# Kernel tuning notes

Hardware: AMD Instinct MI355X
Metric: run time of the kernel (lower is better)

Reference implementation:

```python
import jax, jax.numpy as jnp
import numpy as np

N_NODES = 200000
N_EDGES = 800000
D_IN = 64
D_OUT = 64
NUM_RELATIONS = 16
NUM_BASES = 8


def setup_inputs() -> dict:
    key = jax.random.key(0)
    k_x, k_s, k_t, k_r, k_b, k_a = jax.random.split(key, 6)
    x = jax.random.normal(k_x, (N_NODES, D_IN), dtype=jnp.float32)
    node_keep_mask = jnp.ones((N_NODES,), dtype=bool)
    source = jax.random.randint(k_s, (N_EDGES,), 0, N_NODES, dtype=jnp.int64)
    target = jax.random.randint(k_t, (N_EDGES,), 0, N_NODES, dtype=jnp.int64)
    edge_type = jax.random.randint(k_r, (N_EDGES,), 0, NUM_RELATIONS, dtype=jnp.int64)
    # parameters: xavier-normal bases, L1-normalized attention coefficients
    std = float(np.sqrt(2.0 / (D_IN + D_OUT)))
    bases = jax.random.normal(k_b, (NUM_BASES, D_IN, D_OUT), dtype=jnp.float32) * std
    att = jax.random.uniform(k_a, (NUM_RELATIONS + 1, NUM_BASES), dtype=jnp.float32)
    att = att / jnp.sum(jnp.abs(att), axis=1, keepdims=True)
    return {"x": x, "node_keep_mask": node_keep_mask, "source": source,
            "target": target, "edge_type": edge_type, "bases": bases, "att": att}


def reference(x, node_keep_mask, source, target, edge_type, bases, att):
    num_relations = att.shape[0] - 1
    # per-node, per-basis transformed features: (N, B, D_out)
    t = jnp.einsum('nd,bde->nbe', x, bases)
    # self-loop term (att row num_relations), masked by node_keep_mask
    self_msg = jnp.einsum('nbe,b->ne', t, att[num_relations])
    out = jnp.where(node_keep_mask[:, None], self_msg, jnp.zeros((), dtype=x.dtype))
    # per-node, per-relation messages: (N, R, D_out) -- collapses the per-relation
    # python loop of the original into one contraction
    h = jnp.einsum('nbe,rb->nre', t, att[:num_relations])
    # bidirectional edges (original concatenates [src,tgt] and [tgt,src])
    src2 = jnp.concatenate([source, target])
    tgt2 = jnp.concatenate([target, source])
    et2 = jnp.concatenate([edge_type, edge_type])
    m = h[src2, et2]  # (2E, D_out) gather
    out = out.at[tgt2].add(m)  # scatter-add over edges
    return out
```

## Files before the change

kernel.cpp:

```cpp
#include <hip/hip_runtime.h>
#include <hip/hip_bf16.h>
#include <stdint.h>
#include <stddef.h>

#define N_NODES 200000
#define N_EDGES 800000
#define NREL 16
#define NBASES 8

typedef __attribute__((ext_vector_type(8))) short short8b;
typedef __attribute__((ext_vector_type(4))) float float4v;
typedef __attribute__((ext_vector_type(4))) int int4v;

__device__ __forceinline__ short f32_bf16(float f) {
  uint32_t u = __builtin_bit_cast(uint32_t, f);
  uint32_t r = u + 0x7FFFu + ((u >> 16) & 1u);
  return (short)(uint16_t)(r >> 16);
}
__device__ __forceinline__ uint16_t f32_bf16_hw(float f) {
  __hip_bfloat16 h = __float2bfloat16(f);
  return __builtin_bit_cast(uint16_t, h);
}
__device__ __forceinline__ float bf2f(uint16_t h) {
  return __builtin_bit_cast(float, (uint32_t)h << 16);
}

__global__ __launch_bounds__(256) void k_wprep(const float* __restrict__ bases,
                                               const float* __restrict__ att,
                                               uint16_t* __restrict__ Wt) {
  int i = blockIdx.x * 256 + threadIdx.x;
  if (i >= 17 * 64 * 64) return;
  int r = i >> 12;
  int e = (i >> 6) & 63;
  int d = i & 63;
  float acc = 0.f;
  for (int b = 0; b < NBASES; ++b)
    acc += att[r * NBASES + b] * bases[b * 4096 + d * 64 + e];
  Wt[i] = (uint16_t)f32_bf16(acc);
}

#define MAXTILES 112528
#define MAXRECS  (MAXTILES * 16)
#define NB 196
#define CNT_BLOCKS  782
#define CAST_BLOCKS 6250
#define PREP_BLOCKS 440
#define WS_CNTR    0
#define WS_GCUR2   128
#define WS_RSTART  256
#define WS_GCUR    384
#define WS_WT      512
#define WS_TILEREL 139776
#define WS_VSTART  1052416
#define WS_CNTT    1852416
#define WS_RECS    2652416
#define WS_MSG     17056128
#define WS_TOTAL   (WS_MSG + (size_t)MAXRECS * 128)
#define TR_RELOFF  WS_MSG
#define TR_NOFF    (TR_RELOFF + 3200000)
#define TR_ESLOT   (TR_NOFF + 800000)
#define TR_SCRATCH (TR_ESLOT + 6400000)
#define TR_H       (TR_SCRATCH + 6400000)
#define TR_BASE    (TR_H + 613088)
#define TR_REGS    (TR_BASE + 613088)

__global__ __launch_bounds__(256) void k_init(const float* __restrict__ bases,
                                              const float* __restrict__ att,
                                              uint16_t* __restrict__ Wt,
                                              int* __restrict__ zero0) {
  int b = blockIdx.x;
  int tid = threadIdx.x;
  if (b < 273) {
    int i = b * 256 + tid;
    if (i < 17 * 64 * 64) {
      int r = i >> 12;
      int e = (i >> 6) & 63;
      int d = i & 63;
      float acc = 0.f;
      for (int bb = 0; bb < NBASES; ++bb)
        acc += att[r * NBASES + bb] * bases[bb * 4096 + d * 64 + e];
      Wt[i] = (uint16_t)f32_bf16(acc);
    }
  } else {
    if (tid < 128) zero0[tid] = 0;
  }
}

__global__ __launch_bounds__(256) void k_count(const int* __restrict__ src,
                                               const int* __restrict__ tgt,
                                               const int* __restrict__ et,
                                               const int* __restrict__ mask,
                                               int* __restrict__ cntr,
                                               int* __restrict__ H,
                                               int* __restrict__ reloff,
                                               int* __restrict__ noff,
                                               const float* __restrict__ x,
                                               uint16_t* __restrict__ xb,
                                               int nE, int nN) {
  int b = blockIdx.x;
  int tid = threadIdx.x;
  if (b >= CNT_BLOCKS) {
    int i = (b - CNT_BLOCKS) * 256 + tid;
    const float* xp = x + (size_t)i * 8;
    float4v q0 = __builtin_nontemporal_load((const float4v*)xp);
    float4v q1 = __builtin_nontemporal_load((const float4v*)(xp + 4));
    short8b o;
    o[0] = f32_bf16_hw(q0[0]); o[1] = f32_bf16_hw(q0[1]); o[2] = f32_bf16_hw(q0[2]); o[3] = f32_bf16_hw(q0[3]);
    o[4] = f32_bf16_hw(q1[0]); o[5] = f32_bf16_hw(q1[1]); o[6] = f32_bf16_hw(q1[2]); o[7] = f32_bf16_hw(q1[3]);
    *(short8b*)(xb + (size_t)i * 8) = o;
    return;
  }
  __shared__ int lh[NREL + 1], lbase[NREL + 1];
  __shared__ int bh[NB];
  if (tid <= NREL) lh[tid] = 0;
  if (tid < NB) bh[tid] = 0;
  __syncthreads();
  int base = b * 1024 + tid;
  bool isE[4], isN[4];
  int r4[4], loff[4], loffN[4];
#pragma unroll
  for (int k = 0; k < 4; ++k) {
    int i = base + k * 256;
    isE[k] = i < nE;
    isN[k] = (i < nN) && mask[i];
    if (isE[k]) {
      r4[k] = et[i];
      int s_ = src[i], t_ = tgt[i];
      loff[k] = atomicAdd(&lh[r4[k]], 2);
      atomicAdd(&bh[t_ >> 10], 1);
      atomicAdd(&bh[s_ >> 10], 1);
    }
    if (isN[k]) loffN[k] = atomicAdd(&lh[NREL], 1);
  }
  __syncthreads();
  if (tid <= NREL)
    lbase[tid] = lh[tid] ? atomicAdd(&cntr[tid], lh[tid]) : 0;
  if (tid < NB) H[b * NB + tid] = bh[tid];
  __syncthreads();
#pragma unroll
  for (int k = 0; k < 4; ++k) {
    int i = base + k * 256;
    if (isE[k]) __builtin_nontemporal_store(lbase[r4[k]] + loff[k], reloff + i);
    if (isN[k]) __builtin_nontemporal_store(lbase[NREL] + loffN[k], noff + i);
  }
}

__global__ __launch_bounds__(256) void k_base(const int* __restrict__ H,
                                              int* __restrict__ baseM,
                                              int* __restrict__ regStart,
                                              int* __restrict__ regTot,
                                              int* __restrict__ gcur2,
                                              const int* __restrict__ cntr,
                                              int* __restrict__ rstart_g,
                                              uint8_t* __restrict__ tileRel,
                                              int2* __restrict__ recs,
                                              int maxTiles) {
  int tid = threadIdx.x;
  if (blockIdx.x >= NB) {
    int bp = blockIdx.x - NB;
    __shared__ int s[NREL + 2];
    if (tid == 0) {
      int base = 0;
      for (int r = 0; r <= NREL; ++r) {
        s[r] = base;
        base = (base + cntr[r] + 15) & ~15;
      }
      s[NREL + 1] = base;
    }
    __syncthreads();
    if (bp == 0) {
      if (tid <= NREL + 1) rstart_g[tid] = s[tid];
      for (int w = tid; w < (NREL + 1) * 16; w += 256) {
        int r = w >> 4, j = w & 15;
        int pos = s[r] + cntr[r] + j;
        if (pos < s[r + 1]) recs[pos] = make_int2(-1, -1);
      }
    }
    int t = bp * 256 + tid;
    if (t < maxTiles) {
      int p = t * 16;
      uint8_t rr = 255;
      if (p < s[NREL + 1]) {
        int q = 0;
        for (int k = 1; k <= NREL; ++k)
          if (p >= s[k]) q = k;
        rr = (uint8_t)q;
      }
      tileRel[t] = rr;
    }
    return;
  }
  int b = blockIdx.x;
  int lane = tid & 63, wid = tid >> 6;
  int vals[4]; int ts = 0;
#pragma unroll
  for (int k = 0; k < 4; ++k) {
    int idx = tid * 4 + k;
    vals[k] = (idx < CNT_BLOCKS) ? H[idx * NB + b] : 0;
    ts += vals[k];
  }
  int incl = ts;
  for (int off = 1; off < 64; off <<= 1) {
    int n = __shfl_up(incl, off, 64);
    if (lane >= off) incl += n;
  }
  __shared__ int wsum[4];
  __shared__ int s_start;
  if (lane == 63) wsum[wid] = incl;
  __syncthreads();
  if (tid == 0) {
    int t0 = wsum[0], t1 = wsum[1], t2 = wsum[2], t3 = wsum[3];
    int tot = t0 + t1 + t2 + t3;
    int st = atomicAdd(gcur2, tot);
    regStart[b] = st;
    regTot[b] = tot;
    s_start = st;
    wsum[0] = 0; wsum[1] = t0; wsum[2] = t0 + t1; wsum[3] = t0 + t1 + t2;
  }
  __syncthreads();
  int run = s_start + wsum[wid] + incl - ts;
#pragma unroll
  for (int k = 0; k < 4; ++k) {
    int idx = tid * 4 + k;
    if (idx < CNT_BLOCKS) {
      baseM[idx * NB + b] = run;
      run += vals[k];
    }
  }
}

__global__ __launch_bounds__(256) void k_scat(const int* __restrict__ src,
                                              const int* __restrict__ tgt,
                                              const int* __restrict__ baseM,
                                              int* __restrict__ scratch,
                                              int nE) {
  int b = blockIdx.x;
  int tid = threadIdx.x;
  __shared__ int bh[NB];
  __shared__ int bb[NB];
  if (tid < NB) { bh[tid] = 0; bb[tid] = baseM[b * NB + tid]; }
  __syncthreads();
#pragma unroll
  for (int k = 0; k < 4; ++k) {
    int i = b * 1024 + k * 256 + tid;
    if (i < nE) {
      int t_ = tgt[i], s_ = src[i];
      int offT = atomicAdd(&bh[t_ >> 10], 1);
      scratch[bb[t_ >> 10] + offT] = ((t_ & 1023) << 21) | (2 * i);
      int offS = atomicAdd(&bh[s_ >> 10], 1);
      scratch[bb[s_ >> 10] + offS] = ((s_ & 1023) << 21) | (2 * i + 1);
    }
  }
}

__global__ __launch_bounds__(256) void k_slot(const int* __restrict__ scratch,
                                              const int* __restrict__ regStart,
                                              const int* __restrict__ regTot,
                                              const int* __restrict__ mask,
                                              const int* __restrict__ noff,
                                              const int* __restrict__ rstart,
                                              int* __restrict__ eslot,
                                              int* __restrict__ vstart,
                                              int* __restrict__ cntt,
                                              int* __restrict__ gcur,
                                              int2* __restrict__ recs,
                                              int nN) {
  int b = blockIdx.x;
  int tid = threadIdx.x;
  __shared__ int cnt[1024];
  __shared__ int sabs[1024];
  __shared__ int wsum[4];
  __shared__ int s_base, s_rs16;
#pragma unroll
  for (int k = 0; k < 4; ++k) cnt[tid + k * 256] = 0;
  if (tid == 0) s_rs16 = rstart[NREL];
  __syncthreads();
  int start = regStart[b];
  int tot = regTot[b];
  for (int it = tid; it < tot; it += 256)
    atomicAdd(&cnt[scratch[start + it] >> 21], 1);
  __syncthreads();
  int lane = tid & 63, wid = tid >> 6;
  int vals[4]; int ts = 0;
#pragma unroll
  for (int k = 0; k < 4; ++k) {
    int j = tid * 4 + k;
    int v = b * 1024 + j;
    int m = (v < nN) ? (mask[v] ? 1 : 0) : 0;
    vals[k] = cnt[j] + m;
    ts += vals[k];
  }
  int incl = ts;
  for (int off = 1; off < 64; off <<= 1) {
    int n = __shfl_up(incl, off, 64);
    if (lane >= off) incl += n;
  }
  if (lane == 63) wsum[wid] = incl;
  __syncthreads();
  if (tid == 0) {
    int t0 = wsum[0], t1 = wsum[1], t2 = wsum[2], t3 = wsum[3];
    s_base = atomicAdd(gcur, t0 + t1 + t2 + t3);
    wsum[0] = 0; wsum[1] = t0; wsum[2] = t0 + t1; wsum[3] = t0 + t1 + t2;
  }
  __syncthreads();
  int run = s_base + wsum[wid] + incl - ts;
#pragma unroll
  for (int k = 0; k < 4; ++k) {
    int j = tid * 4 + k;
    sabs[j] = run;
    int v = b * 1024 + j;
    if (v < nN) { vstart[v] = run; cntt[v] = vals[k]; }
    run += vals[k];
  }
  __syncthreads();
  for (int it = tid; it < tot; it += 256) {
    int rec = scratch[start + it];
    int slot = atomicAdd(&sabs[rec >> 21], 1);
    eslot[rec & 0x1FFFFF] = slot;
  }
  __syncthreads();
#pragma unroll
  for (int k = 0; k < 4; ++k) {
    int j = tid * 4 + k;
    int v = b * 1024 + j;
    if (v < nN && mask[v])
      recs[s_rs16 + noff[v]] = make_int2(v, sabs[j]);
  }
}

__global__ __launch_bounds__(256) void k_write(const int* __restrict__ src,
                                               const int* __restrict__ tgt,
                                               const int* __restrict__ et,
                                               const int* __restrict__ reloff,
                                               const int* __restrict__ eslot,
                                               const int* __restrict__ rstart,
                                               int2* __restrict__ recs,
                                               int nE) {
  __shared__ int s_rs[NREL + 1];
  if (threadIdx.x <= NREL) s_rs[threadIdx.x] = rstart[threadIdx.x];
  __syncthreads();
  int i = blockIdx.x * 256 + threadIdx.x;
  if (i < nE) {
    int r = et[i];
    int rl = __builtin_nontemporal_load(reloff + i);
    long long ev = __builtin_nontemporal_load((const long long*)(eslot + 2 * i));
    int s1 = (int)(ev & 0xFFFFFFFFll);
    int s2 = (int)(ev >> 32);
    int s_ = src[i], t_ = tgt[i];
    int pos = s_rs[r] + rl;
    *(int4*)(recs + pos) = make_int4(s_, s1, t_, s2);
  }
}

__global__ __launch_bounds__(256) void k_phaseA(const uint16_t* __restrict__ xb,
                                                const int2* __restrict__ recs,
                                                const uint16_t* __restrict__ Wt,
                                                const uint8_t* __restrict__ tileRel,
                                                uint16_t* __restrict__ msg,
                                                int ntiles) {
  __shared__ uint16_t s_m[4][2][16 * 72];
  __shared__ int s_slot[4][2][16];
  const int wid = threadIdx.x >> 6;
  const int lane = threadIdx.x & 63;
  const int quad = lane >> 4;
  const int m16 = lane & 15;
  const int t0 = (blockIdx.x * 4 + wid) * 4;

  if (tileRel[t0] == 255) return;

  int rel4[4];
#pragma unroll
  for (int it = 0; it < 4; ++it) {
    int t = t0 + it;
    rel4[it] = (t < ntiles) ? (int)tileRel[t] : 255;
  }
  int2 rec4[4];
#pragma unroll
  for (int it = 0; it < 4; ++it) {
    if (rel4[it] != 255) {
      long long rv = __builtin_nontemporal_load((const long long*)(recs + (t0 + it) * 16 + m16));
      rec4[it].x = (int)(rv & 0xFFFFFFFFll);
      rec4[it].y = (int)(rv >> 32);
    } else {
      rec4[it] = make_int2(-1, -1);
    }
  }
  short8b a0_[4], a1_[4];
#pragma unroll
  for (int it = 0; it < 4; ++it) {
    int u = rec4[it].x < 0 ? 0 : rec4[it].x;
    const uint16_t* xp = xb + (size_t)u * 64 + quad * 8;
    a0_[it] = *(const short8b*)(xp);
    a1_[it] = *(const short8b*)(xp + 32);
  }

  int curRel = -1;
  short8b bfrag[4][2] = {};

#pragma unroll
  for (int it = 0; it < 4; ++it) {
    int rel = rel4[it];
    if (rel == 255) continue;
    int par = it & 1;

    if (rel != curRel) {
      curRel = rel;
      const uint16_t* wbase = Wt + (size_t)rel * 4096;
      for (int nt = 0; nt < 4; ++nt)
        for (int kt = 0; kt < 2; ++kt)
          bfrag[nt][kt] = *(const short8b*)(wbase + (size_t)(nt * 16 + m16) * 64 + kt * 32 + quad * 8);
    }

    float4v acc[4];
    for (int nt = 0; nt < 4; ++nt) { acc[nt][0] = 0.f; acc[nt][1] = 0.f; acc[nt][2] = 0.f; acc[nt][3] = 0.f; }
    for (int nt = 0; nt < 4; ++nt) {
      acc[nt] = __builtin_amdgcn_mfma_f32_16x16x32_bf16(a0_[it], bfrag[nt][0], acc[nt], 0, 0, 0);
      acc[nt] = __builtin_amdgcn_mfma_f32_16x16x32_bf16(a1_[it], bfrag[nt][1], acc[nt], 0, 0, 0);
    }

    if (quad == 0) s_slot[wid][par][m16] = rec4[it].y;
    for (int reg = 0; reg < 4; ++reg)
      for (int nt = 0; nt < 4; ++nt)
        s_m[wid][par][(quad * 4 + reg) * 72 + nt * 16 + m16] = f32_bf16_hw(acc[nt][reg]);

    asm volatile("s_waitcnt lgkmcnt(0)" ::: "memory");
    __builtin_amdgcn_sched_barrier(0);

    for (int p = 0; p < 2; ++p) {
      int row = (lane >> 3) + p * 8;
      int slot = s_slot[wid][par][row];
      if (slot >= 0) {
        const uint16_t* lp = &s_m[wid][par][row * 72 + (lane & 7) * 8];
        int4v val = *(const int4v*)lp;
        __builtin_nontemporal_store(val, (int4v*)(msg + (size_t)slot * 64 + (lane & 7) * 8));
      }
    }
  }
}

__global__ __launch_bounds__(256) void k_phaseB(const uint16_t* __restrict__ msg,
                                                const int* __restrict__ cntt,
                                                const int* __restrict__ vstart,
                                                float* __restrict__ out, int nN) {
  int v = blockIdx.x * 32 + (threadIdx.x >> 3);
  int l = threadIdx.x & 7;
  if (v >= nN) return;
  int cnt = cntt[v];
  int base = vstart[v];
  float a[8] = {0.f, 0.f, 0.f, 0.f, 0.f, 0.f, 0.f, 0.f};
  const uint16_t* mp = msg + (size_t)base * 64 + l * 8;
  int j = 0;
  for (; j + 2 <= cnt; j += 2) {
    int4v r0 = __builtin_nontemporal_load((const int4v*)(mp + (size_t)j * 64));
    int4v r1 = __builtin_nontemporal_load((const int4v*)(mp + (size_t)(j + 1) * 64));
    short8b h0 = __builtin_bit_cast(short8b, r0);
    short8b h1 = __builtin_bit_cast(short8b, r1);
#pragma unroll
    for (int k = 0; k < 8; ++k)
      a[k] += bf2f((uint16_t)h0[k]) + bf2f((uint16_t)h1[k]);
  }
  if (j < cnt) {
    int4v r0 = __builtin_nontemporal_load((const int4v*)(mp + (size_t)j * 64));
    short8b h = __builtin_bit_cast(short8b, r0);
#pragma unroll
    for (int k = 0; k < 8; ++k)
      a[k] += bf2f((uint16_t)h[k]);
  }
  float* op = out + (size_t)v * 64 + l * 8;
  float4v o0, o1;
  o0[0] = a[0]; o0[1] = a[1]; o0[2] = a[2]; o0[3] = a[3];
  o1[0] = a[4]; o1[1] = a[5]; o1[2] = a[6]; o1[3] = a[7];
  __builtin_nontemporal_store(o0, (float4v*)op);
  __builtin_nontemporal_store(o1, (float4v*)(op + 4));
}

#define F_WS_HIST    0
#define F_WS_CURSOR  64
#define F_WS_START   128
#define F_WS_WT      512
#define F_WS_TILEREL 139776
#define F_WS_RECS    262144
#define F_MAXTILES   112520
#define F_MAXRECS    (F_MAXTILES * 16)

__global__ __launch_bounds__(256) void f_hist(const int* __restrict__ et,
                                              int* __restrict__ hist, int nE) {
  __shared__ int lh[NREL];
  if (threadIdx.x < NREL) lh[threadIdx.x] = 0;
  __syncthreads();
  int i = blockIdx.x * 256 + threadIdx.x;
  if (i < nE) atomicAdd(&lh[et[i]], 2);
  __syncthreads();
  if (threadIdx.x < NREL && lh[threadIdx.x] > 0)
    atomicAdd(&hist[threadIdx.x], lh[threadIdx.x]);
}

__global__ __launch_bounds__(256) void f_prefix(const int* __restrict__ hist,
                                                int* __restrict__ cursor,
                                                int* __restrict__ start,
                                                uint8_t* __restrict__ tileRel,
                                                int nN, int maxTiles) {
  __shared__ int s_start[17];
  if (threadIdx.x == 0) {
    int base = nN;
    for (int r = 0; r < NREL; ++r) {
      s_start[r] = base;
      cursor[r] = base;
      start[r] = base;
      base = (base + hist[r] + 15) & ~15;
    }
    s_start[16] = base;
    start[16] = base;
  }
  __syncthreads();
  int endp = s_start[16];
  for (int t = threadIdx.x; t < maxTiles; t += 256) {
    int p = t * 16;
    uint8_t r;
    if (p < nN) r = 16;
    else if (p >= endp) r = 255;
    else {
      int q = 0;
      for (int k = 1; k < NREL; ++k) if (p >= s_start[k]) q = k;
      r = (uint8_t)q;
    }
    tileRel[t] = r;
  }
}

__global__ __launch_bounds__(256) void f_scatter(const int* __restrict__ src,
                                                 const int* __restrict__ tgt,
                                                 const int* __restrict__ et,
                                                 const int* __restrict__ mask,
                                                 int2* __restrict__ recs,
                                                 int* __restrict__ cursor,
                                                 int nE, int nN) {
  __shared__ int lh[NREL];
  __shared__ int lbase[NREL];
  if (threadIdx.x < NREL) lh[threadIdx.x] = 0;
  __syncthreads();
  int i = blockIdx.x * 256 + threadIdx.x;
  int r = 0, loff = 0;
  bool isEdge = (i < nE);
  if (isEdge) {
    r = et[i];
    loff = atomicAdd(&lh[r], 2);
  }
  __syncthreads();
  if (threadIdx.x < NREL)
    lbase[threadIdx.x] = (lh[threadIdx.x] > 0) ? atomicAdd(&cursor[threadIdx.x], lh[threadIdx.x]) : 0;
  __syncthreads();
  if (isEdge) {
    int pos = lbase[r] + loff;
    int s = src[i], t = tgt[i];
    *(int4*)(recs + pos) = make_int4(s, t, t, s);
  }
  if (i < nN) {
    recs[i] = (mask[i] != 0) ? make_int2(i, i) : make_int2(-1, -1);
  }
}

__global__ __launch_bounds__(256) void f_compute(const float* __restrict__ x,
                                                 const int2* __restrict__ recs,
                                                 const uint16_t* __restrict__ Wt,
                                                 const uint8_t* __restrict__ tileRel,
                                                 float* __restrict__ out,
                                                 int ntiles) {
  const int lane = threadIdx.x & 63;
  const int quad = lane >> 4;
  const int m16 = lane & 15;
  const int wave = blockIdx.x * 4 + (threadIdx.x >> 6);
  const int t0 = wave * 4;

  int curRel = -1;
  short8b bfrag[4][2] = {};

  for (int it = 0; it < 4; ++it) {
    int t = t0 + it;
    if (t >= ntiles) return;
    int rel = tileRel[t];
    if (rel == 255) return;

    if (rel != curRel) {
      curRel = rel;
      const uint16_t* wbase = Wt + (size_t)rel * 4096;
      for (int nt = 0; nt < 4; ++nt)
        for (int kt = 0; kt < 2; ++kt)
          bfrag[nt][kt] = *(const short8b*)(wbase + (size_t)(nt * 16 + m16) * 64 + kt * 32 + quad * 8);
    }

    int2 rec = recs[t * 16 + m16];
    int u = rec.x < 0 ? 0 : rec.x;

    const float* xp = x + (size_t)u * 64 + quad * 8;
    float4v q0 = *(const float4v*)(xp);
    float4v q1 = *(const float4v*)(xp + 4);
    float4v q2 = *(const float4v*)(xp + 32);
    float4v q3 = *(const float4v*)(xp + 36);
    short8b a0, a1;
    a0[0] = f32_bf16(q0[0]); a0[1] = f32_bf16(q0[1]); a0[2] = f32_bf16(q0[2]); a0[3] = f32_bf16(q0[3]);
    a0[4] = f32_bf16(q1[0]); a0[5] = f32_bf16(q1[1]); a0[6] = f32_bf16(q1[2]); a0[7] = f32_bf16(q1[3]);
    a1[0] = f32_bf16(q2[0]); a1[1] = f32_bf16(q2[1]); a1[2] = f32_bf16(q2[2]); a1[3] = f32_bf16(q2[3]);
    a1[4] = f32_bf16(q3[0]); a1[5] = f32_bf16(q3[1]); a1[6] = f32_bf16(q3[2]); a1[7] = f32_bf16(q3[3]);

    float4v acc[4];
    for (int nt = 0; nt < 4; ++nt) { acc[nt][0] = 0.f; acc[nt][1] = 0.f; acc[nt][2] = 0.f; acc[nt][3] = 0.f; }
    for (int nt = 0; nt < 4; ++nt) {
      acc[nt] = __builtin_amdgcn_mfma_f32_16x16x32_bf16(a0, bfrag[nt][0], acc[nt], 0, 0, 0);
      acc[nt] = __builtin_amdgcn_mfma_f32_16x16x32_bf16(a1, bfrag[nt][1], acc[nt], 0, 0, 0);
    }

    int tg[4];
    for (int reg = 0; reg < 4; ++reg)
      tg[reg] = __shfl(rec.y, quad * 4 + reg, 64);
    for (int reg = 0; reg < 4; ++reg) {
      if (tg[reg] < 0) continue;
      float* op = out + (size_t)tg[reg] * 64 + m16;
      for (int nt = 0; nt < 4; ++nt)
        __hip_atomic_fetch_add(op + nt * 16, acc[nt][reg], __ATOMIC_RELAXED, __HIP_MEMORY_SCOPE_AGENT);
    }
  }
}

extern "C" void kernel_launch(void* const* d_in, const int* in_sizes, int n_in,
                              void* d_out, int out_size, void* d_ws, size_t ws_size,
                              hipStream_t stream) {
  const float* x     = (const float*)d_in[0];
  const int*   mask  = (const int*)d_in[1];
  const int*   src   = (const int*)d_in[2];
  const int*   tgt   = (const int*)d_in[3];
  const int*   et    = (const int*)d_in[4];
  const float* bases = (const float*)d_in[5];
  const float* att   = (const float*)d_in[6];
  float* out = (float*)d_out;
  char* ws = (char*)d_ws;

  if (ws_size >= WS_TOTAL) {
    int*      cntr    = (int*)(ws + WS_CNTR);
    int*      gcur2   = (int*)(ws + WS_GCUR2);
    int*      rstart  = (int*)(ws + WS_RSTART);
    int*      gcur    = (int*)(ws + WS_GCUR);
    uint16_t* Wt      = (uint16_t*)(ws + WS_WT);
    uint8_t*  tileRel = (uint8_t*)(ws + WS_TILEREL);
    int*      vstart  = (int*)(ws + WS_VSTART);
    int*      cntt    = (int*)(ws + WS_CNTT);
    int2*     recs    = (int2*)(ws + WS_RECS);
    uint16_t* msg     = (uint16_t*)(ws + WS_MSG);
    int*      reloff  = (int*)(ws + TR_RELOFF);
    int*      noff    = (int*)(ws + TR_NOFF);
    int*      eslot   = (int*)(ws + TR_ESLOT);
    int*      scratch = (int*)(ws + TR_SCRATCH);
    int*      H       = (int*)(ws + TR_H);
    int*      baseM   = (int*)(ws + TR_BASE);
    int*      regStart= (int*)(ws + TR_REGS);
    int*      regTot  = regStart + NB;
    uint16_t* xb      = (uint16_t*)out;

    k_init<<<274, 256, 0, stream>>>(bases, att, Wt, (int*)ws);
    k_count<<<CNT_BLOCKS + CAST_BLOCKS, 256, 0, stream>>>(src, tgt, et, mask, cntr, H, reloff, noff, x, xb, N_EDGES, N_NODES);
    k_base<<<NB + PREP_BLOCKS, 256, 0, stream>>>(H, baseM, regStart, regTot, gcur2, cntr, rstart, tileRel, recs, MAXTILES);
    k_scat<<<CNT_BLOCKS, 256, 0, stream>>>(src, tgt, baseM, scratch, N_EDGES);
    k_slot<<<NB, 256, 0, stream>>>(scratch, regStart, regTot, mask, noff, rstart, eslot, vstart, cntt, gcur, recs, N_NODES);
    k_write<<<(N_EDGES + 255) / 256, 256, 0, stream>>>(src, tgt, et, reloff, eslot, rstart, recs, N_EDGES);
    k_phaseA<<<(MAXTILES + 15) / 16, 256, 0, stream>>>(xb, recs, Wt, tileRel, msg, MAXTILES);
    k_phaseB<<<(N_NODES + 31) / 32, 256, 0, stream>>>(msg, cntt, vstart, out, N_NODES);
  } else {
    int*      hist    = (int*)(ws + F_WS_HIST);
    int*      cursor  = (int*)(ws + F_WS_CURSOR);
    int*      start   = (int*)(ws + F_WS_START);
    uint16_t* Wt      = (uint16_t*)(ws + F_WS_WT);
    uint8_t*  tileRel = (uint8_t*)(ws + F_WS_TILEREL);
    int2*     recs    = (int2*)(ws + F_WS_RECS);

    (void)hipMemsetAsync(out, 0, (size_t)N_NODES * 64 * sizeof(float), stream);
    (void)hipMemsetAsync(ws, 0, 512, stream);
    (void)hipMemsetAsync(recs, 0xFF, (size_t)F_MAXRECS * sizeof(int2), stream);

    k_wprep<<<(17 * 64 * 64 + 255) / 256, 256, 0, stream>>>(bases, att, Wt);
    f_hist<<<(N_EDGES + 255) / 256, 256, 0, stream>>>(et, hist, N_EDGES);
    f_prefix<<<1, 256, 0, stream>>>(hist, cursor, start, tileRel, N_NODES, F_MAXTILES);
    f_scatter<<<(N_EDGES + 255) / 256, 256, 0, stream>>>(src, tgt, et, mask, recs, cursor, N_EDGES, N_NODES);
    f_compute<<<(F_MAXTILES + 15) / 16, 256, 0, stream>>>(x, recs, Wt, tileRel, out, F_MAXTILES);
  }
}
```

Measured before the change: 298.8 us.

## Aggregate att-weighted inputs per node then apply bases in one fused GEMM

Reorders the contraction: each target node first gathers its neighbours' bf16 features and accumulates them into an 8-basis vector weighted by the per-relation attention coefficients, including the self-loop. A single MFMA GEMM against the bases then produces the output. This replaces the per-edge, per-relation message GEMM, the large bf16 message buffer written and reread by the old two-phase path, and the relation-bucketing kernels. In exchange the gather loop runs serially per node and is latency-bound, and the aggregated basis vector is rounded to bf16 before the GEMM.

```diff
diff --git a/kernel.cpp b/kernel.cpp
--- a/kernel.cpp
+++ b/kernel.cpp
@@ -24,6 +24,309 @@
 __device__ __forceinline__ float bf2f(uint16_t h) {
   return __builtin_bit_cast(float, (uint32_t)h << 16);
 }
+
+#define NB 196
+#define CNT_BLOCKS  782
+#define CAST_BLOCKS 6250
+#define MAXSLOTS (2 * N_EDGES + N_NODES)
+
+#define WS_GCUR2   128
+#define WS_GCUR    384
+#define WS_BT      512
+#define WS_VSTART  66560
+#define WS_CNTT    866560
+#define WS_ESLOT   1666560
+#define WS_SCRATCH 8066560
+#define WS_H       14466560
+#define WS_BASEM   15079648
+#define WS_REGS    15692736
+#define WS_REC2    15694336
+#define WS_XB      30094336
+#define WS_GATE    (17056128 + (size_t)112528 * 16 * 128)
+
+__global__ __launch_bounds__(256) void k_init(const float* __restrict__ bases,
+                                              uint16_t* __restrict__ Bt,
+                                              int* __restrict__ zero0) {
+  int b = blockIdx.x;
+  int tid = threadIdx.x;
+  if (b < 128) {
+    int i = b * 256 + tid;
+    int e = i >> 9;
+    int bb = (i >> 6) & 7;
+    int d = i & 63;
+    Bt[i] = f32_bf16_hw(bases[bb * 4096 + d * 64 + e]);
+  } else {
+    if (tid < 128) zero0[tid] = 0;
+  }
+}
+
+__global__ __launch_bounds__(256) void k_count(const int* __restrict__ src,
+                                               const int* __restrict__ tgt,
+                                               int* __restrict__ H,
+                                               const float* __restrict__ x,
+                                               uint16_t* __restrict__ xb,
+                                               int nE) {
+  int b = blockIdx.x;
+  int tid = threadIdx.x;
+  if (b >= CNT_BLOCKS) {
+    int i = (b - CNT_BLOCKS) * 256 + tid;
+    const float* xp = x + (size_t)i * 8;
+    float4v q0 = __builtin_nontemporal_load((const float4v*)xp);
+    float4v q1 = __builtin_nontemporal_load((const float4v*)(xp + 4));
+    short8b o;
+    o[0] = f32_bf16_hw(q0[0]); o[1] = f32_bf16_hw(q0[1]); o[2] = f32_bf16_hw(q0[2]); o[3] = f32_bf16_hw(q0[3]);
+    o[4] = f32_bf16_hw(q1[0]); o[5] = f32_bf16_hw(q1[1]); o[6] = f32_bf16_hw(q1[2]); o[7] = f32_bf16_hw(q1[3]);
+    *(short8b*)(xb + (size_t)i * 8) = o;
+    return;
+  }
+  __shared__ int bh[NB];
+  if (tid < NB) bh[tid] = 0;
+  __syncthreads();
+#pragma unroll
+  for (int k = 0; k < 4; ++k) {
+    int i = b * 1024 + k * 256 + tid;
+    if (i < nE) {
+      atomicAdd(&bh[tgt[i] >> 10], 1);
+      atomicAdd(&bh[src[i] >> 10], 1);
+    }
+  }
+  __syncthreads();
+  if (tid < NB) H[b * NB + tid] = bh[tid];
+}
+
+__global__ __launch_bounds__(256) void k_base(const int* __restrict__ H,
+                                              int* __restrict__ baseM,
+                                              int* __restrict__ regStart,
+                                              int* __restrict__ regTot,
+                                              int* __restrict__ gcur2) {
+  int b = blockIdx.x;
+  int tid = threadIdx.x;
+  int lane = tid & 63, wid = tid >> 6;
+  int vals[4]; int ts = 0;
+#pragma unroll
+  for (int k = 0; k < 4; ++k) {
+    int idx = tid * 4 + k;
+    vals[k] = (idx < CNT_BLOCKS) ? H[idx * NB + b] : 0;
+    ts += vals[k];
+  }
+  int incl = ts;
+  for (int off = 1; off < 64; off <<= 1) {
+    int n = __shfl_up(incl, off, 64);
+    if (lane >= off) incl += n;
+  }
+  __shared__ int wsum[4];
+  __shared__ int s_start;
+  if (lane == 63) wsum[wid] = incl;
+  __syncthreads();
+  if (tid == 0) {
+    int t0 = wsum[0], t1 = wsum[1], t2 = wsum[2], t3 = wsum[3];
+    int tot = t0 + t1 + t2 + t3;
+    int st = atomicAdd(gcur2, tot);
+    regStart[b] = st;
+    regTot[b] = tot;
+    s_start = st;
+    wsum[0] = 0; wsum[1] = t0; wsum[2] = t0 + t1; wsum[3] = t0 + t1 + t2;
+  }
+  __syncthreads();
+  int run = s_start + wsum[wid] + incl - ts;
+#pragma unroll
+  for (int k = 0; k < 4; ++k) {
+    int idx = tid * 4 + k;
+    if (idx < CNT_BLOCKS) {
+      baseM[idx * NB + b] = run;
+      run += vals[k];
+    }
+  }
+}
+
+__global__ __launch_bounds__(256) void k_scat(const int* __restrict__ src,
+                                              const int* __restrict__ tgt,
+                                              const int* __restrict__ baseM,
+                                              int* __restrict__ scratch,
+                                              int nE) {
+  int b = blockIdx.x;
+  int tid = threadIdx.x;
+  __shared__ int bh[NB];
+  __shared__ int bb[NB];
+  if (tid < NB) { bh[tid] = 0; bb[tid] = baseM[b * NB + tid]; }
+  __syncthreads();
+#pragma unroll
+  for (int k = 0; k < 4; ++k) {
+    int i = b * 1024 + k * 256 + tid;
+    if (i < nE) {
+      int t_ = tgt[i], s_ = src[i];
+      int offT = atomicAdd(&bh[t_ >> 10], 1);
+      scratch[bb[t_ >> 10] + offT] = ((t_ & 1023) << 21) | (2 * i);
+      int offS = atomicAdd(&bh[s_ >> 10], 1);
+      scratch[bb[s_ >> 10] + offS] = ((s_ & 1023) << 21) | (2 * i + 1);
+    }
+  }
+}
+
+__global__ __launch_bounds__(256) void k_slot(const int* __restrict__ scratch,
+                                              const int* __restrict__ regStart,
+                                              const int* __restrict__ regTot,
+                                              const int* __restrict__ mask,
+                                              int* __restrict__ eslot,
+                                              int* __restrict__ vstart,
+                                              int* __restrict__ cntt,
+                                              int* __restrict__ gcur,
+                                              int2* __restrict__ rec2,
+                                              int nN) {
+  int b = blockIdx.x;
+  int tid = threadIdx.x;
+  __shared__ int cnt[1024];
+  __shared__ int sabs[1024];
+  __shared__ int wsum[4];
+  __shared__ int s_base;
+#pragma unroll
+  for (int k = 0; k < 4; ++k) cnt[tid + k * 256] = 0;
+  __syncthreads();
+  int start = regStart[b];
+  int tot = regTot[b];
+  for (int it = tid; it < tot; it += 256)
+    atomicAdd(&cnt[scratch[start + it] >> 21], 1);
+  __syncthreads();
+  int lane = tid & 63, wid = tid >> 6;
+  int vals[4]; int ts = 0;
+#pragma unroll
+  for (int k = 0; k < 4; ++k) {
+    int j = tid * 4 + k;
+    int v = b * 1024 + j;
+    int m = (v < nN) ? (mask[v] ? 1 : 0) : 0;
+    vals[k] = cnt[j] + m;
+    ts += vals[k];
+  }
+  int incl = ts;
+  for (int off = 1; off < 64; off <<= 1) {
+    int n = __shfl_up(incl, off, 64);
+    if (lane >= off) incl += n;
+  }
+  if (lane == 63) wsum[wid] = incl;
+  __syncthreads();
+  if (tid == 0) {
+    int t0 = wsum[0], t1 = wsum[1], t2 = wsum[2], t3 = wsum[3];
+    s_base = atomicAdd(gcur, t0 + t1 + t2 + t3);
+    wsum[0] = 0; wsum[1] = t0; wsum[2] = t0 + t1; wsum[3] = t0 + t1 + t2;
+  }
+  __syncthreads();
+  int run = s_base + wsum[wid] + incl - ts;
+#pragma unroll
+  for (int k = 0; k < 4; ++k) {
+    int j = tid * 4 + k;
+    sabs[j] = run;
+    int v = b * 1024 + j;
+    if (v < nN) { vstart[v] = run; cntt[v] = vals[k]; }
+    run += vals[k];
+  }
+  __syncthreads();
+  for (int it = tid; it < tot; it += 256) {
+    int rec = scratch[start + it];
+    int slot = atomicAdd(&sabs[rec >> 21], 1);
+    eslot[rec & 0x1FFFFF] = slot;
+  }
+  __syncthreads();
+#pragma unroll
+  for (int k = 0; k < 4; ++k) {
+    int j = tid * 4 + k;
+    int v = b * 1024 + j;
+    if (v < nN && mask[v])
+      rec2[sabs[j]] = make_int2(v, NREL);
+  }
+}
+
+__global__ __launch_bounds__(256) void k_write(const int* __restrict__ src,
+                                               const int* __restrict__ tgt,
+                                               const int* __restrict__ et,
+                                               const int* __restrict__ eslot,
+                                               int2* __restrict__ rec2,
+                                               int nE) {
+  int i = blockIdx.x * 256 + threadIdx.x;
+  if (i < nE) {
+    int r = et[i];
+    long long ev = __builtin_nontemporal_load((const long long*)(eslot + 2 * i));
+    int s1 = (int)(ev & 0xFFFFFFFFll);
+    int s2 = (int)(ev >> 32);
+    int s_ = src[i], t_ = tgt[i];
+    rec2[s1] = make_int2(s_, r);
+    rec2[s2] = make_int2(t_, r);
+  }
+}
+
+__global__ __launch_bounds__(256) void k_phaseAB(const uint16_t* __restrict__ xb,
+                                                 const int2* __restrict__ rec2,
+                                                 const uint16_t* __restrict__ Bt,
+                                                 const float* __restrict__ att,
+                                                 const int* __restrict__ vstart,
+                                                 const int* __restrict__ cntt,
+                                                 float* __restrict__ out) {
+  __shared__ __align__(16) uint16_t s_g[16 * 520];
+  __shared__ float s_att[(NREL + 1) * NBASES];
+  int tid = threadIdx.x;
+  if (tid < (NREL + 1) * NBASES) s_att[tid] = att[tid];
+  int wv = tid >> 6;
+  int lane = tid & 63;
+  int T0 = blockIdx.x * 16;
+
+  int tb[4], tc[4];
+#pragma unroll
+  for (int tt = 0; tt < 4; ++tt) {
+    int t = T0 + wv * 4 + tt;
+    tb[tt] = vstart[t];
+    tc[tt] = cntt[t];
+  }
+  __syncthreads();
+
+  float g[4][8] = {};
+  int mx = max(max(tc[0], tc[1]), max(tc[2], tc[3]));
+  for (int j = 0; j < mx; ++j) {
+#pragma unroll
+    for (int tt = 0; tt < 4; ++tt) {
+      if (j < tc[tt]) {
+        int2 rc = rec2[tb[tt] + j];
+        float xv = bf2f(xb[(size_t)rc.x * 64 + lane]);
+        const float* ar = &s_att[rc.y * 8];
+#pragma unroll
+        for (int bb = 0; bb < 8; ++bb)
+          g[tt][bb] = fmaf(ar[bb], xv, g[tt][bb]);
+      }
+    }
+  }
+#pragma unroll
+  for (int tt = 0; tt < 4; ++tt) {
+    int row = wv * 4 + tt;
+#pragma unroll
+    for (int bb = 0; bb < 8; ++bb)
+      s_g[row * 520 + bb * 64 + lane] = f32_bf16_hw(g[tt][bb]);
+  }
+  __syncthreads();
+
+  int quad = lane >> 4, m16 = lane & 15;
+  float4v acc0 = {0.f, 0.f, 0.f, 0.f}, acc1 = {0.f, 0.f, 0.f, 0.f};
+  const uint16_t* bt = Bt + (size_t)(wv * 16 + m16) * 512 + quad * 8;
+  const uint16_t* ga = &s_g[m16 * 520 + quad * 8];
+#pragma unroll
+  for (int kk = 0; kk < 16; kk += 2) {
+    short8b a0 = *(const short8b*)(ga + kk * 32);
+    short8b b0 = *(const short8b*)(bt + kk * 32);
+    acc0 = __builtin_amdgcn_mfma_f32_16x16x32_bf16(a0, b0, acc0, 0, 0, 0);
+    short8b a1 = *(const short8b*)(ga + (kk + 1) * 32);
+    short8b b1 = *(const short8b*)(bt + (kk + 1) * 32);
+    acc1 = __builtin_amdgcn_mfma_f32_16x16x32_bf16(a1, b1, acc1, 0, 0, 0);
+  }
+#pragma unroll
+  for (int reg = 0; reg < 4; ++reg)
+    out[(size_t)(T0 + quad * 4 + reg) * 64 + wv * 16 + m16] = acc0[reg] + acc1[reg];
+}
+
+#define F_WS_HIST    0
+#define F_WS_CURSOR  64
+#define F_WS_START   128
+#define F_WS_WT      512
+#define F_WS_TILEREL 139776
+#define F_WS_RECS    262144
+#define F_MAXTILES   112520
+#define F_MAXRECS    (F_MAXTILES * 16)
 
 __global__ __launch_bounds__(256) void k_wprep(const float* __restrict__ bases,
                                                const float* __restrict__ att,
@@ -38,450 +341,6 @@
     acc += att[r * NBASES + b] * bases[b * 4096 + d * 64 + e];
   Wt[i] = (uint16_t)f32_bf16(acc);
 }
-
-#define MAXTILES 112528
-#define MAXRECS  (MAXTILES * 16)
-#define NB 196
-#define CNT_BLOCKS  782
-#define CAST_BLOCKS 6250
-#define PREP_BLOCKS 440
-#define WS_CNTR    0
-#define WS_GCUR2   128
-#define WS_RSTART  256
-#define WS_GCUR    384
-#define WS_WT      512
-#define WS_TILEREL 139776
-#define WS_VSTART  1052416
-#define WS_CNTT    1852416
-#define WS_RECS    2652416
-#define WS_MSG     17056128
-#define WS_TOTAL   (WS_MSG + (size_t)MAXRECS * 128)
-#define TR_RELOFF  WS_MSG
-#define TR_NOFF    (TR_RELOFF + 3200000)
-#define TR_ESLOT   (TR_NOFF + 800000)
-#define TR_SCRATCH (TR_ESLOT + 6400000)
-#define TR_H       (TR_SCRATCH + 6400000)
-#define TR_BASE    (TR_H + 613088)
-#define TR_REGS    (TR_BASE + 613088)
-
-__global__ __launch_bounds__(256) void k_init(const float* __restrict__ bases,
-                                              const float* __restrict__ att,
-                                              uint16_t* __restrict__ Wt,
-                                              int* __restrict__ zero0) {
-  int b = blockIdx.x;
-  int tid = threadIdx.x;
-  if (b < 273) {
-    int i = b * 256 + tid;
-    if (i < 17 * 64 * 64) {
-      int r = i >> 12;
-      int e = (i >> 6) & 63;
-      int d = i & 63;
-      float acc = 0.f;
-      for (int bb = 0; bb < NBASES; ++bb)
-        acc += att[r * NBASES + bb] * bases[bb * 4096 + d * 64 + e];
-      Wt[i] = (uint16_t)f32_bf16(acc);
-    }
-  } else {
-    if (tid < 128) zero0[tid] = 0;
-  }
-}
-
-__global__ __launch_bounds__(256) void k_count(const int* __restrict__ src,
-                                               const int* __restrict__ tgt,
-                                               const int* __restrict__ et,
-                                               const int* __restrict__ mask,
-                                               int* __restrict__ cntr,
-                                               int* __restrict__ H,
-                                               int* __restrict__ reloff,
-                                               int* __restrict__ noff,
-                                               const float* __restrict__ x,
-                                               uint16_t* __restrict__ xb,
-                                               int nE, int nN) {
-  int b = blockIdx.x;
-  int tid = threadIdx.x;
-  if (b >= CNT_BLOCKS) {
-    int i = (b - CNT_BLOCKS) * 256 + tid;
-    const float* xp = x + (size_t)i * 8;
-    float4v q0 = __builtin_nontemporal_load((const float4v*)xp);
-    float4v q1 = __builtin_nontemporal_load((const float4v*)(xp + 4));
-    short8b o;
-    o[0] = f32_bf16_hw(q0[0]); o[1] = f32_bf16_hw(q0[1]); o[2] = f32_bf16_hw(q0[2]); o[3] = f32_bf16_hw(q0[3]);
-    o[4] = f32_bf16_hw(q1[0]); o[5] = f32_bf16_hw(q1[1]); o[6] = f32_bf16_hw(q1[2]); o[7] = f32_bf16_hw(q1[3]);
-    *(short8b*)(xb + (size_t)i * 8) = o;
-    return;
-  }
-  __shared__ int lh[NREL + 1], lbase[NREL + 1];
-  __shared__ int bh[NB];
-  if (tid <= NREL) lh[tid] = 0;
-  if (tid < NB) bh[tid] = 0;
-  __syncthreads();
-  int base = b * 1024 + tid;
-  bool isE[4], isN[4];
-  int r4[4], loff[4], loffN[4];
-#pragma unroll
-  for (int k = 0; k < 4; ++k) {
-    int i = base + k * 256;
-    isE[k] = i < nE;
-    isN[k] = (i < nN) && mask[i];
-    if (isE[k]) {
-      r4[k] = et[i];
-      int s_ = src[i], t_ = tgt[i];
-      loff[k] = atomicAdd(&lh[r4[k]], 2);
-      atomicAdd(&bh[t_ >> 10], 1);
-      atomicAdd(&bh[s_ >> 10], 1);
-    }
-    if (isN[k]) loffN[k] = atomicAdd(&lh[NREL], 1);
-  }
-  __syncthreads();
-  if (tid <= NREL)
-    lbase[tid] = lh[tid] ? atomicAdd(&cntr[tid], lh[tid]) : 0;
-  if (tid < NB) H[b * NB + tid] = bh[tid];
-  __syncthreads();
-#pragma unroll
-  for (int k = 0; k < 4; ++k) {
-    int i = base + k * 256;
-    if (isE[k]) __builtin_nontemporal_store(lbase[r4[k]] + loff[k], reloff + i);
-    if (isN[k]) __builtin_nontemporal_store(lbase[NREL] + loffN[k], noff + i);
-  }
-}
-
-__global__ __launch_bounds__(256) void k_base(const int* __restrict__ H,
-                                              int* __restrict__ baseM,
-                                              int* __restrict__ regStart,
-                                              int* __restrict__ regTot,
-                                              int* __restrict__ gcur2,
-                                              const int* __restrict__ cntr,
-                                              int* __restrict__ rstart_g,
-                                              uint8_t* __restrict__ tileRel,
-                                              int2* __restrict__ recs,
-                                              int maxTiles) {
-  int tid = threadIdx.x;
-  if (blockIdx.x >= NB) {
-    int bp = blockIdx.x - NB;
-    __shared__ int s[NREL + 2];
-    if (tid == 0) {
-      int base = 0;
-      for (int r = 0; r <= NREL; ++r) {
-        s[r] = base;
-        base = (base + cntr[r] + 15) & ~15;
-      }
-      s[NREL + 1] = base;
-    }
-    __syncthreads();
-    if (bp == 0) {
-      if (tid <= NREL + 1) rstart_g[tid] = s[tid];
-      for (int w = tid; w < (NREL + 1) * 16; w += 256) {
-        int r = w >> 4, j = w & 15;
-        int pos = s[r] + cntr[r] + j;
-        if (pos < s[r + 1]) recs[pos] = make_int2(-1, -1);
-      }
-    }
-    int t = bp * 256 + tid;
-    if (t < maxTiles) {
-      int p = t * 16;
-      uint8_t rr = 255;
-      if (p < s[NREL + 1]) {
-        int q = 0;
-        for (int k = 1; k <= NREL; ++k)
-          if (p >= s[k]) q = k;
-        rr = (uint8_t)q;
-      }
-      tileRel[t] = rr;
-    }
-    return;
-  }
-  int b = blockIdx.x;
-  int lane = tid & 63, wid = tid >> 6;
-  int vals[4]; int ts = 0;
-#pragma unroll
-  for (int k = 0; k < 4; ++k) {
-    int idx = tid * 4 + k;
-    vals[k] = (idx < CNT_BLOCKS) ? H[idx * NB + b] : 0;
-    ts += vals[k];
-  }
-  int incl = ts;
-  for (int off = 1; off < 64; off <<= 1) {
-    int n = __shfl_up(incl, off, 64);
-    if (lane >= off) incl += n;
-  }
-  __shared__ int wsum[4];
-  __shared__ int s_start;
-  if (lane == 63) wsum[wid] = incl;
-  __syncthreads();
-  if (tid == 0) {
-    int t0 = wsum[0], t1 = wsum[1], t2 = wsum[2], t3 = wsum[3];
-    int tot = t0 + t1 + t2 + t3;
-    int st = atomicAdd(gcur2, tot);
-    regStart[b] = st;
-    regTot[b] = tot;
-    s_start = st;
-    wsum[0] = 0; wsum[1] = t0; wsum[2] = t0 + t1; wsum[3] = t0 + t1 + t2;
-  }
-  __syncthreads();
-  int run = s_start + wsum[wid] + incl - ts;
-#pragma unroll
-  for (int k = 0; k < 4; ++k) {
-    int idx = tid * 4 + k;
-    if (idx < CNT_BLOCKS) {
-      baseM[idx * NB + b] = run;
-      run += vals[k];
-    }
-  }
-}
-
-__global__ __launch_bounds__(256) void k_scat(const int* __restrict__ src,
-                                              const int* __restrict__ tgt,
-                                              const int* __restrict__ baseM,
-                                              int* __restrict__ scratch,
-                                              int nE) {
-  int b = blockIdx.x;
-  int tid = threadIdx.x;
-  __shared__ int bh[NB];
-  __shared__ int bb[NB];
-  if (tid < NB) { bh[tid] = 0; bb[tid] = baseM[b * NB + tid]; }
-  __syncthreads();
-#pragma unroll
-  for (int k = 0; k < 4; ++k) {
-    int i = b * 1024 + k * 256 + tid;
-    if (i < nE) {
-      int t_ = tgt[i], s_ = src[i];
-      int offT = atomicAdd(&bh[t_ >> 10], 1);
-      scratch[bb[t_ >> 10] + offT] = ((t_ & 1023) << 21) | (2 * i);
-      int offS = atomicAdd(&bh[s_ >> 10], 1);
-      scratch[bb[s_ >> 10] + offS] = ((s_ & 1023) << 21) | (2 * i + 1);
-    }
-  }
-}
-
-__global__ __launch_bounds__(256) void k_slot(const int* __restrict__ scratch,
-                                              const int* __restrict__ regStart,
-                                              const int* __restrict__ regTot,
-                                              const int* __restrict__ mask,
-                                              const int* __restrict__ noff,
-                                              const int* __restrict__ rstart,
-                                              int* __restrict__ eslot,
-                                              int* __restrict__ vstart,
-                                              int* __restrict__ cntt,
-                                              int* __restrict__ gcur,
-                                              int2* __restrict__ recs,
-                                              int nN) {
-  int b = blockIdx.x;
-  int tid = threadIdx.x;
-  __shared__ int cnt[1024];
-  __shared__ int sabs[1024];
-  __shared__ int wsum[4];
-  __shared__ int s_base, s_rs16;
-#pragma unroll
-  for (int k = 0; k < 4; ++k) cnt[tid + k * 256] = 0;
-  if (tid == 0) s_rs16 = rstart[NREL];
-  __syncthreads();
-  int start = regStart[b];
-  int tot = regTot[b];
-  for (int it = tid; it < tot; it += 256)
-    atomicAdd(&cnt[scratch[start + it] >> 21], 1);
-  __syncthreads();
-  int lane = tid & 63, wid = tid >> 6;
-  int vals[4]; int ts = 0;
-#pragma unroll
-  for (int k = 0; k < 4; ++k) {
-    int j = tid * 4 + k;
-    int v = b * 1024 + j;
-    int m = (v < nN) ? (mask[v] ? 1 : 0) : 0;
-    vals[k] = cnt[j] + m;
-    ts += vals[k];
-  }
-  int incl = ts;
-  for (int off = 1; off < 64; off <<= 1) {
-    int n = __shfl_up(incl, off, 64);
-    if (lane >= off) incl += n;
-  }
-  if (lane == 63) wsum[wid] = incl;
-  __syncthreads();
-  if (tid == 0) {
-    int t0 = wsum[0], t1 = wsum[1], t2 = wsum[2], t3 = wsum[3];
-    s_base = atomicAdd(gcur, t0 + t1 + t2 + t3);
-    wsum[0] = 0; wsum[1] = t0; wsum[2] = t0 + t1; wsum[3] = t0 + t1 + t2;
-  }
-  __syncthreads();
-  int run = s_base + wsum[wid] + incl - ts;
-#pragma unroll
-  for (int k = 0; k < 4; ++k) {
-    int j = tid * 4 + k;
-    sabs[j] = run;
-    int v = b * 1024 + j;
-    if (v < nN) { vstart[v] = run; cntt[v] = vals[k]; }
-    run += vals[k];
-  }
-  __syncthreads();
-  for (int it = tid; it < tot; it += 256) {
-    int rec = scratch[start + it];
-    int slot = atomicAdd(&sabs[rec >> 21], 1);
-    eslot[rec & 0x1FFFFF] = slot;
-  }
-  __syncthreads();
-#pragma unroll
-  for (int k = 0; k < 4; ++k) {
-    int j = tid * 4 + k;
-    int v = b * 1024 + j;
-    if (v < nN && mask[v])
-      recs[s_rs16 + noff[v]] = make_int2(v, sabs[j]);
-  }
-}
-
-__global__ __launch_bounds__(256) void k_write(const int* __restrict__ src,
-                                               const int* __restrict__ tgt,
-                                               const int* __restrict__ et,
-                                               const int* __restrict__ reloff,
-                                               const int* __restrict__ eslot,
-                                               const int* __restrict__ rstart,
-                                               int2* __restrict__ recs,
-                                               int nE) {
-  __shared__ int s_rs[NREL + 1];
-  if (threadIdx.x <= NREL) s_rs[threadIdx.x] = rstart[threadIdx.x];
-  __syncthreads();
-  int i = blockIdx.x * 256 + threadIdx.x;
-  if (i < nE) {
-    int r = et[i];
-    int rl = __builtin_nontemporal_load(reloff + i);
-    long long ev = __builtin_nontemporal_load((const long long*)(eslot + 2 * i));
-    int s1 = (int)(ev & 0xFFFFFFFFll);
-    int s2 = (int)(ev >> 32);
-    int s_ = src[i], t_ = tgt[i];
-    int pos = s_rs[r] + rl;
-    *(int4*)(recs + pos) = make_int4(s_, s1, t_, s2);
-  }
-}
-
-__global__ __launch_bounds__(256) void k_phaseA(const uint16_t* __restrict__ xb,
-                                                const int2* __restrict__ recs,
-                                                const uint16_t* __restrict__ Wt,
-                                                const uint8_t* __restrict__ tileRel,
-                                                uint16_t* __restrict__ msg,
-                                                int ntiles) {
-  __shared__ uint16_t s_m[4][2][16 * 72];
-  __shared__ int s_slot[4][2][16];
-  const int wid = threadIdx.x >> 6;
-  const int lane = threadIdx.x & 63;
-  const int quad = lane >> 4;
-  const int m16 = lane & 15;
-  const int t0 = (blockIdx.x * 4 + wid) * 4;
-
-  if (tileRel[t0] == 255) return;
-
-  int rel4[4];
-#pragma unroll
-  for (int it = 0; it < 4; ++it) {
-    int t = t0 + it;
-    rel4[it] = (t < ntiles) ? (int)tileRel[t] : 255;
-  }
-  int2 rec4[4];
-#pragma unroll
-  for (int it = 0; it < 4; ++it) {
-    if (rel4[it] != 255) {
-      long long rv = __builtin_nontemporal_load((const long long*)(recs + (t0 + it) * 16 + m16));
-      rec4[it].x = (int)(rv & 0xFFFFFFFFll);
-      rec4[it].y = (int)(rv >> 32);
-    } else {
-      rec4[it] = make_int2(-1, -1);
-    }
-  }
-  short8b a0_[4], a1_[4];
-#pragma unroll
-  for (int it = 0; it < 4; ++it) {
-    int u = rec4[it].x < 0 ? 0 : rec4[it].x;
-    const uint16_t* xp = xb + (size_t)u * 64 + quad * 8;
-    a0_[it] = *(const short8b*)(xp);
-    a1_[it] = *(const short8b*)(xp + 32);
-  }
-
-  int curRel = -1;
-  short8b bfrag[4][2] = {};
-
-#pragma unroll
-  for (int it = 0; it < 4; ++it) {
-    int rel = rel4[it];
-    if (rel == 255) continue;
-    int par = it & 1;
-
-    if (rel != curRel) {
-      curRel = rel;
-      const uint16_t* wbase = Wt + (size_t)rel * 4096;
-      for (int nt = 0; nt < 4; ++nt)
-        for (int kt = 0; kt < 2; ++kt)
-          bfrag[nt][kt] = *(const short8b*)(wbase + (size_t)(nt * 16 + m16) * 64 + kt * 32 + quad * 8);
-    }
-
-    float4v acc[4];
-    for (int nt = 0; nt < 4; ++nt) { acc[nt][0] = 0.f; acc[nt][1] = 0.f; acc[nt][2] = 0.f; acc[nt][3] = 0.f; }
-    for (int nt = 0; nt < 4; ++nt) {
-      acc[nt] = __builtin_amdgcn_mfma_f32_16x16x32_bf16(a0_[it], bfrag[nt][0], acc[nt], 0, 0, 0);
-      acc[nt] = __builtin_amdgcn_mfma_f32_16x16x32_bf16(a1_[it], bfrag[nt][1], acc[nt], 0, 0, 0);
-    }
-
-    if (quad == 0) s_slot[wid][par][m16] = rec4[it].y;
-    for (int reg = 0; reg < 4; ++reg)
-      for (int nt = 0; nt < 4; ++nt)
-        s_m[wid][par][(quad * 4 + reg) * 72 + nt * 16 + m16] = f32_bf16_hw(acc[nt][reg]);
-
-    asm volatile("s_waitcnt lgkmcnt(0)" ::: "memory");
-    __builtin_amdgcn_sched_barrier(0);
-
-    for (int p = 0; p < 2; ++p) {
-      int row = (lane >> 3) + p * 8;
-      int slot = s_slot[wid][par][row];
-      if (slot >= 0) {
-        const uint16_t* lp = &s_m[wid][par][row * 72 + (lane & 7) * 8];
-        int4v val = *(const int4v*)lp;
-        __builtin_nontemporal_store(val, (int4v*)(msg + (size_t)slot * 64 + (lane & 7) * 8));
-      }
-    }
-  }
-}
-
-__global__ __launch_bounds__(256) void k_phaseB(const uint16_t* __restrict__ msg,
-                                                const int* __restrict__ cntt,
-                                                const int* __restrict__ vstart,
-                                                float* __restrict__ out, int nN) {
-  int v = blockIdx.x * 32 + (threadIdx.x >> 3);
-  int l = threadIdx.x & 7;
-  if (v >= nN) return;
-  int cnt = cntt[v];
-  int base = vstart[v];
-  float a[8] = {0.f, 0.f, 0.f, 0.f, 0.f, 0.f, 0.f, 0.f};
-  const uint16_t* mp = msg + (size_t)base * 64 + l * 8;
-  int j = 0;
-  for (; j + 2 <= cnt; j += 2) {
-    int4v r0 = __builtin_nontemporal_load((const int4v*)(mp + (size_t)j * 64));
-    int4v r1 = __builtin_nontemporal_load((const int4v*)(mp + (size_t)(j + 1) * 64));
-    short8b h0 = __builtin_bit_cast(short8b, r0);
-    short8b h1 = __builtin_bit_cast(short8b, r1);
-#pragma unroll
-    for (int k = 0; k < 8; ++k)
-      a[k] += bf2f((uint16_t)h0[k]) + bf2f((uint16_t)h1[k]);
-  }
-  if (j < cnt) {
-    int4v r0 = __builtin_nontemporal_load((const int4v*)(mp + (size_t)j * 64));
-    short8b h = __builtin_bit_cast(short8b, r0);
-#pragma unroll
-    for (int k = 0; k < 8; ++k)
-      a[k] += bf2f((uint16_t)h[k]);
-  }
-  float* op = out + (size_t)v * 64 + l * 8;
-  float4v o0, o1;
-  o0[0] = a[0]; o0[1] = a[1]; o0[2] = a[2]; o0[3] = a[3];
-  o1[0] = a[4]; o1[1] = a[5]; o1[2] = a[6]; o1[3] = a[7];
-  __builtin_nontemporal_store(o0, (float4v*)op);
-  __builtin_nontemporal_store(o1, (float4v*)(op + 4));
-}
-
-#define F_WS_HIST    0
-#define F_WS_CURSOR  64
-#define F_WS_START   128
-#define F_WS_WT      512
-#define F_WS_TILEREL 139776
-#define F_WS_RECS    262144
-#define F_MAXTILES   112520
-#define F_MAXRECS    (F_MAXTILES * 16)
 
 __global__ __launch_bounds__(256) void f_hist(const int* __restrict__ et,
                                               int* __restrict__ hist, int nE) {
@@ -635,35 +494,28 @@
   float* out = (float*)d_out;
   char* ws = (char*)d_ws;
 
-  if (ws_size >= WS_TOTAL) {
-    int*      cntr    = (int*)(ws + WS_CNTR);
+  if (ws_size >= WS_GATE) {
     int*      gcur2   = (int*)(ws + WS_GCUR2);
-    int*      rstart  = (int*)(ws + WS_RSTART);
     int*      gcur    = (int*)(ws + WS_GCUR);
-    uint16_t* Wt      = (uint16_t*)(ws + WS_WT);
-    uint8_t*  tileRel = (uint8_t*)(ws + WS_TILEREL);
+    uint16_t* Bt      = (uint16_t*)(ws + WS_BT);
     int*      vstart  = (int*)(ws + WS_VSTART);
     int*      cntt    = (int*)(ws + WS_CNTT);
-    int2*     recs    = (int2*)(ws + WS_RECS);
-    uint16_t* msg     = (uint16_t*)(ws + WS_MSG);
-    int*      reloff  = (int*)(ws + TR_RELOFF);
-    int*      noff    = (int*)(ws + TR_NOFF);
-    int*      eslot   = (int*)(ws + TR_ESLOT);
-    int*      scratch = (int*)(ws + TR_SCRATCH);
-    int*      H       = (int*)(ws + TR_H);
-    int*      baseM   = (int*)(ws + TR_BASE);
-    int*      regStart= (int*)(ws + TR_REGS);
+    int*      eslot   = (int*)(ws + WS_ESLOT);
+    int*      scratch = (int*)(ws + WS_SCRATCH);
+    int*      H       = (int*)(ws + WS_H);
+    int*      baseM   = (int*)(ws + WS_BASEM);
+    int*      regStart= (int*)(ws + WS_REGS);
     int*      regTot  = regStart + NB;
-    uint16_t* xb      = (uint16_t*)out;
-
-    k_init<<<274, 256, 0, stream>>>(bases, att, Wt, (int*)ws);
-    k_count<<<CNT_BLOCKS + CAST_BLOCKS, 256, 0, stream>>>(src, tgt, et, mask, cntr, H, reloff, noff, x, xb, N_EDGES, N_NODES);
-    k_base<<<NB + PREP_BLOCKS, 256, 0, stream>>>(H, baseM, regStart, regTot, gcur2, cntr, rstart, tileRel, recs, MAXTILES);
+    int2*     rec2    = (int2*)(ws + WS_REC2);
+    uint16_t* xb      = (uint16_t*)(ws + WS_XB);
+
+    k_init<<<129, 256, 0, stream>>>(bases, Bt, (int*)ws);
+    k_count<<<CNT_BLOCKS + CAST_BLOCKS, 256, 0, stream>>>(src, tgt, H, x, xb, N_EDGES);
+    k_base<<<NB, 256, 0, stream>>>(H, baseM, regStart, regTot, gcur2);
     k_scat<<<CNT_BLOCKS, 256, 0, stream>>>(src, tgt, baseM, scratch, N_EDGES);
-    k_slot<<<NB, 256, 0, stream>>>(scratch, regStart, regTot, mask, noff, rstart, eslot, vstart, cntt, gcur, recs, N_NODES);
-    k_write<<<(N_EDGES + 255) / 256, 256, 0, stream>>>(src, tgt, et, reloff, eslot, rstart, recs, N_EDGES);
-    k_phaseA<<<(MAXTILES + 15) / 16, 256, 0, stream>>>(xb, recs, Wt, tileRel, msg, MAXTILES);
-    k_phaseB<<<(N_NODES + 31) / 32, 256, 0, stream>>>(msg, cntt, vstart, out, N_NODES);
+    k_slot<<<NB, 256, 0, stream>>>(scratch, regStart, regTot, mask, eslot, vstart, cntt, gcur, rec2, N_NODES);
+    k_write<<<(N_EDGES + 255) / 256, 256, 0, stream>>>(src, tgt, et, eslot, rec2, N_EDGES);
+    k_phaseAB<<<N_NODES / 16, 256, 0, stream>>>(xb, rec2, Bt, att, vstart, cntt, out);
   } else {
     int*      hist    = (int*)(ws + F_WS_HIST);
     int*      cursor  = (int*)(ws + F_WS_CURSOR);
```

Result: slower. 443.4 us (+48.4%).
